# Performance work log

Hardware: AMD Instinct MI355X
Metric: run time of the kernel (lower is better)

## Reference

```python
import jax, jax.numpy as jnp
import numpy as np
from jax import lax

BATCH = 2
COUNT = 5
OUT = 125


def _bins(n, out=OUT):
    # PyTorch adaptive_max_pool2d bin boundaries: start=floor(i*n/out), end=ceil((i+1)*n/out)
    i = np.arange(out)
    s = (i * n) // out
    e = -((-(i + 1) * n) // out)
    m = int((e - s).max())
    idx = s[:, None] + np.arange(m)[None, :]
    return np.minimum(idx, n - 1), idx < e[:, None]


def _apool(img):
    # adaptive max pool 2d of [H,W] -> [OUT,OUT]; H,W are concrete Python ints
    H, W = img.shape
    ri, rv = _bins(H)
    ci, cv = _bins(W)
    r = jnp.where(rv[:, :, None], img[ri], -jnp.inf).max(axis=1)       # [OUT, W]
    return jnp.where(cv[None], r[:, ci], -jnp.inf).max(axis=2)         # [OUT, OUT]


def _conv(x, w, b):
    y = lax.conv_general_dilated(x, w, (1, 1), 'VALID', dimension_numbers=('NCHW', 'OIHW', 'NCHW'))
    return y + b[None, :, None, None]


def _bn(x, g, be, m, v):
    inv = g * lax.rsqrt(v + 1e-5)
    return x * inv[None, :, None, None] + (be - m * inv)[None, :, None, None]


def _pool(x, k, s):
    return lax.reduce_window(x, -np.inf, lax.max, (1, 1, k, k), (1, 1, s, s), 'VALID')


def _forward(x, ROI, roi_layer, w1, b1, g1, be1, m1, v1, w2, b2, g2, be2, m2, v2,
             w3, b3, g3, be3, m3, v3, w4, b4, g4, be4, m4, v4, fw1, fb1, fw2, fb2, fw3, fb3):
    ROI = np.asarray(ROI)
    rl = int(roi_layer)
    roiX = jax.nn.relu(_bn(_conv(x, w1, b1), g1, be1, m1, v1))  # [2,3,252,252]
    crops = []
    for k in range(BATCH):
        xs = []
        for j in range(rl):
            for i in range(COUNT):
                y1, y2, x1, x2 = (int(v) for v in ROI[k, i, 0])
                y1 = int(y1 * 0.9); y2 = int(y2 * 0.9); x2 = int(x2 * 0.9); x1 = int(x1 * 0.9)
                xs.append(_apool(roiX[k, j, y1:y2, x1:x2]))
        crops.append(xs)
    # original code prepends each batch's crop list -> batch order reversed; .numpy() detaches grads
    xb = lax.stop_gradient(jnp.stack(crops[1] + crops[0]).reshape(BATCH, COUNT * rl, OUT, OUT))
    norX = _pool(jax.nn.relu(_bn(_conv(x, w2, b2), g2, be2, m2, v2)), 4, 2)  # [2,20,125,125]
    h = jnp.concatenate([norX, xb], axis=1)                                   # [2,35,125,125]
    h = _pool(jax.nn.relu(_bn(_conv(h, w3, b3), g3, be3, m3, v3)), 2, 2)      # [2,50,60,60]
    h = _pool(jax.nn.relu(_bn(_conv(h, w4, b4), g4, be4, m4, v4)), 2, 2)      # [2,25,28,28]
    h = h.reshape(BATCH, -1)                                                  # [2,19600]
    h = jax.nn.relu(h @ fw1 + fb1)
    h = jax.nn.relu(h @ fw2 + fb2)
    h = jax.nn.relu(h @ fw3 + fb3)
    return jax.nn.softmax(h, axis=1)


def setup_inputs() -> dict:
    key = jax.random.key(0)
    ks = jax.random.split(key, 8)
    rng = np.random.default_rng(0)
    y1 = rng.integers(0, 100, (BATCH, COUNT))
    y2 = np.minimum(y1 + rng.integers(60, 150, (BATCH, COUNT)), 251)
    x1 = rng.integers(0, 100, (BATCH, COUNT))
    x2 = np.minimum(x1 + rng.integers(60, 150, (BATCH, COUNT)), 251)
    ROI = jnp.asarray(np.stack([y1, y2, x1, x2], -1)[:, :, None, :].astype(np.int32))
    d = {'x': jax.random.normal(ks[0], (BATCH, 1, 256, 256), jnp.float32), 'ROI': ROI, 'roi_layer': 3}
    d.update(w1=jax.random.normal(ks[1], (3, 1, 5, 5)) * 0.05, b1=jnp.zeros(3), g1=jnp.ones(3), be1=jnp.zeros(3), m1=jnp.zeros(3), v1=jnp.ones(3))
    d.update(w2=jax.random.normal(ks[2], (20, 1, 5, 5)) * 0.05, b2=jnp.zeros(20), g2=jnp.ones(20), be2=jnp.zeros(20), m2=jnp.zeros(20), v2=jnp.ones(20))
    d.update(w3=jax.random.normal(ks[3], (50, 35, 5, 5)) * 0.05, b3=jnp.zeros(50), g3=jnp.ones(50), be3=jnp.zeros(50), m3=jnp.zeros(50), v3=jnp.ones(50))
    d.update(w4=jax.random.normal(ks[4], (25, 50, 5, 5)) * 0.05, b4=jnp.zeros(25), g4=jnp.ones(25), be4=jnp.zeros(25), m4=jnp.zeros(25), v4=jnp.ones(25))
    d.update(fw1=jax.random.normal(ks[5], (25 * 28 * 28, 1024)) * 0.01, fb1=jnp.zeros(1024),
             fw2=jax.random.normal(ks[6], (1024, 32)) * 0.05, fb2=jnp.zeros(32),
             fw3=jax.random.normal(ks[7], (32, 2)) * 0.05, fb3=jnp.zeros(2))
    return d


def reference(x, ROI, roi_layer, w1, b1, g1, be1, m1, v1, w2, b2, g2, be2, m2, v2,
              w3, b3, g3, be3, m3, v3, w4, b4, g4, be4, m4, v4, fw1, fb1, fw2, fb2, fw3, fb3):
    return _forward(x, ROI, roi_layer, w1, b1, g1, be1, m1, v1, w2, b2, g2, be2, m2, v2,
                    w3, b3, g3, be3, m3, v3, w4, b4, g4, be4, m4, v4, fw1, fb1, fw2, fb2, fw3, fb3)
```

## Files before the change

kernel.cpp:

```cpp
#include <hip/hip_runtime.h>
#include <math.h>


#define RL 3
#define NCH 35

__global__ __launch_bounds__(256) void conv2_roi(
    const float* __restrict__ x, const int* __restrict__ ROI,
    const float* __restrict__ w2, const float* __restrict__ b2, const float* __restrict__ g2,
    const float* __restrict__ be2, const float* __restrict__ m2, const float* __restrict__ v2,
    const float* __restrict__ w1, const float* __restrict__ b1, const float* __restrict__ g1,
    const float* __restrict__ be1, const float* __restrict__ m1, const float* __restrict__ v1,
    float* __restrict__ h1) {
    int i = blockIdx.x * 256 + threadIdx.x;
    if (i >= 125 * 125) return;
    int oy = i / 125, ox = i % 125;
    if (blockIdx.y < 40) {
        int c = blockIdx.y % 20;
        int bi = blockIdx.y / 20;
        const float* xp = x + bi * 256 * 256 + (2 * oy) * 256 + 2 * ox;
        float wl[25];
#pragma unroll
        for (int k = 0; k < 25; k++) wl[k] = w2[c * 25 + k];
        float in[8][8];
#pragma unroll
        for (int r = 0; r < 8; r++)
#pragma unroll
            for (int k = 0; k < 4; k++) {
                float2 v2v = *(const float2*)(xp + r * 256 + 2 * k);
                in[r][2 * k] = v2v.x;
                in[r][2 * k + 1] = v2v.y;
            }
        float inv = g2[c] * rsqrtf(v2[c] + 1e-5f);
        float sh = (b2[c] - m2[c]) * inv + be2[c];
        float mx = -INFINITY;
#pragma unroll
        for (int py = 0; py < 4; py++) {
#pragma unroll
            for (int px = 0; px < 4; px++) {
                float acc = 0.f;
#pragma unroll
                for (int ky = 0; ky < 5; ky++)
#pragma unroll
                    for (int kx = 0; kx < 5; kx++)
                        acc = fmaf(in[py + ky][px + kx], wl[ky * 5 + kx], acc);
                mx = fmaxf(mx, fmaxf(acc * inv + sh, 0.f));
            }
        }
        h1[((bi * NCH + c) * 125 + oy) * 125 + ox] = mx;
    } else {
        int yz = blockIdx.y - 40;
        int bi = yz / 15;
        int cc = yz % 15;
        int sb = 1 - bi;
        int j = cc / 5;
        int ri = cc % 5;
        const int* rp = ROI + (sb * 5 + ri) * 4;
        int y1 = (9 * rp[0]) / 10;
        int y2 = (9 * rp[1]) / 10;
        int x1 = (9 * rp[2]) / 10;
        int x2 = (9 * rp[3]) / 10;
        int H = y2 - y1;
        int W = x2 - x1;
        int sy = (oy * H) / 125, ey = ((oy + 1) * H + 124) / 125;
        int sx = (ox * W) / 125, ex = ((ox + 1) * W + 124) / 125;
        float wl[25];
#pragma unroll
        for (int k = 0; k < 25; k++) wl[k] = w1[j * 25 + k];
        float inv = g1[j] * rsqrtf(v1[j] + 1e-5f);
        float sh = (b1[j] - m1[j]) * inv + be1[j];
        const float* xp = x + sb * 256 * 256;
        float mx = -INFINITY;
        for (int r = sy; r < ey; r++) {
            for (int c2 = sx; c2 < ex; c2++) {
                int Y = y1 + r, X = x1 + c2;
                float acc = 0.f;
#pragma unroll
                for (int ky = 0; ky < 5; ky++)
#pragma unroll
                    for (int kx = 0; kx < 5; kx++)
                        acc = fmaf(xp[(Y + ky) * 256 + X + kx], wl[ky * 5 + kx], acc);
                mx = fmaxf(mx, fmaxf(acc * inv + sh, 0.f));
            }
        }
        h1[((bi * NCH + 20 + cc) * 125 + oy) * 125 + ox] = mx;
    }
}

template <int IW, int PO, int CI, int CO, int G, int NG, int NS>
__global__ __launch_bounds__(64) void conv_partial(
    const float* __restrict__ in, const float* __restrict__ w,
    float* __restrict__ pac) {
    __shared__ float tile[2][20][24];

    const int lane = threadIdx.x;
    const int sy = lane >> 3, sx = lane & 7;
    int z = blockIdx.z;
    const int ng = z % NG; z /= NG;
    const int s = z % NS;
    const int bi = z / NS;
    const int co0 = ng * G;
    constexpr int CPS = (CI + NS - 1) / NS;
    const int ci0 = s * CPS;
    const int ci1 = (ci0 + CPS < CI) ? ci0 + CPS : CI;
    const int px0 = (8 * (int)blockIdx.x < PO - 8) ? 8 * (int)blockIdx.x : PO - 8;
    const int py0 = (8 * (int)blockIdx.y < PO - 8) ? 8 * (int)blockIdx.y : PO - 8;
    const int px = px0 + sx, py = py0 + sy;
    const float* ip = in + (size_t)bi * CI * IW * IW + (size_t)(2 * py0) * IW + 2 * px0;

    int cw[G];
#pragma unroll
    for (int gg = 0; gg < G; gg++) cw[gg] = (co0 + gg < CO) ? co0 + gg : CO - 1;

    float2 sreg[4];
    auto loadstage = [&](int ci) {
        const float* src = ip + (size_t)ci * IW * IW;
#pragma unroll
        for (int k = 0; k < 4; k++) {
            int p = lane + k * 64;
            if (p < 200) {
                int r = p / 10, c2 = (p % 10) * 2;
                sreg[k] = *(const float2*)(src + r * IW + c2);
            }
        }
    };
    auto writestage = [&](int buf) {
#pragma unroll
        for (int k = 0; k < 4; k++) {
            int p = lane + k * 64;
            if (p < 200) {
                int r = p / 10, c2 = (p % 10) * 2;
                *(float2*)&tile[buf][r][c2] = sreg[k];
            }
        }
    };

    loadstage(ci0);
    writestage(0);
    float acc[G][4];
#pragma unroll
    for (int gg = 0; gg < G; gg++)
#pragma unroll
        for (int q = 0; q < 4; q++) acc[gg][q] = 0.f;

    for (int ci = ci0; ci < ci1; ci++) {
        const int cur = (ci - ci0) & 1;
        if (ci + 1 < ci1) loadstage(ci + 1);
        float2 p[6][3];
#pragma unroll
        for (int r = 0; r < 6; r++)
#pragma unroll
            for (int c = 0; c < 3; c++)
                p[r][c] = *(const float2*)&tile[cur][2 * sy + r][2 * sx + 2 * c];
#define E(r, cc) (((cc) & 1) ? p[r][(cc) >> 1].y : p[r][(cc) >> 1].x)
#pragma unroll
        for (int gg = 0; gg < G; gg++) {
            const float* wk = w + ((size_t)cw[gg] * CI + ci) * 25;
#pragma unroll
            for (int ky = 0; ky < 5; ky++) {
#pragma unroll
                for (int kx = 0; kx < 5; kx++) {
                    float wv = wk[ky * 5 + kx];
                    acc[gg][0] = fmaf(E(ky, kx), wv, acc[gg][0]);
                    acc[gg][1] = fmaf(E(ky, kx + 1), wv, acc[gg][1]);
                    acc[gg][2] = fmaf(E(ky + 1, kx), wv, acc[gg][2]);
                    acc[gg][3] = fmaf(E(ky + 1, kx + 1), wv, acc[gg][3]);
                }
            }
        }
#undef E
        if (ci + 1 < ci1) writestage(cur ^ 1);
    }

    constexpr int CW = 2 * PO;
#pragma unroll
    for (int gg = 0; gg < G; gg++) {
        int co = co0 + gg;
        if (co < CO) {
            size_t base = (((size_t)(s * 2 + bi) * CO + co) * CW + 2 * py) * CW + 2 * px;
            float2 r0 = {acc[gg][0], acc[gg][1]};
            float2 r1 = {acc[gg][2], acc[gg][3]};
            *(float2*)&pac[base] = r0;
            *(float2*)&pac[base + CW] = r1;
        }
    }
}

template <int PO, int CO, int NS, int INIT>
__global__ __launch_bounds__(256) void conv_finish(
    const float* __restrict__ pac,
    const float* __restrict__ b, const float* __restrict__ g,
    const float* __restrict__ be, const float* __restrict__ m,
    const float* __restrict__ v, float* __restrict__ out,
    const float* __restrict__ fb1, float* __restrict__ fc1o) {
    int idx = blockIdx.x * 256 + threadIdx.x;
    if (INIT && idx < 2048) fc1o[idx] = fb1[idx & 1023];
    int total = 2 * CO * PO * PO;
    if (idx >= total) return;
    int px = idx % PO;
    int t = idx / PO;
    int py = t % PO; t /= PO;
    int co = t % CO;
    int bi = t / CO;
    constexpr int CW = 2 * PO;
    constexpr size_t SS = (size_t)2 * CO * CW * CW;
    size_t base = (((size_t)bi * CO + co) * CW + 2 * py) * CW + 2 * px;
    float s00 = 0.f, s01 = 0.f, s10 = 0.f, s11 = 0.f;
#pragma unroll
    for (int s = 0; s < NS; s++) {
        float2 a0 = *(const float2*)&pac[base + s * SS];
        float2 a1 = *(const float2*)&pac[base + s * SS + CW];
        s00 += a0.x; s01 += a0.y; s10 += a1.x; s11 += a1.y;
    }
    float inv = g[co] * rsqrtf(v[co] + 1e-5f);
    float sh = (b[co] - m[co]) * inv + be[co];
    float q0 = fmaxf(s00 * inv + sh, 0.f);
    float q1 = fmaxf(s01 * inv + sh, 0.f);
    float q2 = fmaxf(s10 * inv + sh, 0.f);
    float q3 = fmaxf(s11 * inv + sh, 0.f);
    out[idx] = fmaxf(fmaxf(q0, q1), fmaxf(q2, q3));
}

#define CHUNK 50
__global__ void fc1_mm(const float* __restrict__ h, const float* __restrict__ w,
                       float* __restrict__ out) {
    __shared__ float sh[2][CHUNK];
    int o = blockIdx.x * 256 + threadIdx.x;
    int i0 = blockIdx.y * CHUNK;
    if (threadIdx.x < 2 * CHUNK) {
        int r = threadIdx.x / CHUNK, t = threadIdx.x % CHUNK;
        sh[r][t] = h[r * 19600 + i0 + t];
    }
    __syncthreads();
    float a0 = 0.f, a1 = 0.f;
    const float* wp = w + (size_t)i0 * 1024 + o;
#pragma unroll
    for (int i = 0; i < CHUNK; i++) {
        float wv = wp[(size_t)i * 1024];
        a0 = fmaf(sh[0][i], wv, a0);
        a1 = fmaf(sh[1][i], wv, a1);
    }
    atomicAdd(&out[o], a0);
    atomicAdd(&out[1024 + o], a1);
}

__global__ void head(const float* __restrict__ fc1o, const float* __restrict__ fw2,
                     const float* __restrict__ fb2, const float* __restrict__ fw3,
                     const float* __restrict__ fb3, float* __restrict__ out) {
    int bi = blockIdx.x;
    __shared__ float h[1024];
    __shared__ float red[256];
    __shared__ float s2[32];
    for (int i = threadIdx.x; i < 1024; i += 256) h[i] = fmaxf(fc1o[bi * 1024 + i], 0.f);
    __syncthreads();
    int o = threadIdx.x >> 3;
    int part = threadIdx.x & 7;
    float a = 0.f;
    for (int i = part * 128; i < part * 128 + 128; i++) a += h[i] * fw2[i * 32 + o];
    red[threadIdx.x] = a;
    __syncthreads();
    if (part == 0) {
        float s = 0.f;
        for (int p = 0; p < 8; p++) s += red[(o << 3) + p];
        s2[o] = fmaxf(s + fb2[o], 0.f);
    }
    __syncthreads();
    if (threadIdx.x == 0) {
        float z0 = fb3[0], z1 = fb3[1];
        for (int i = 0; i < 32; i++) {
            z0 += s2[i] * fw3[i * 2];
            z1 += s2[i] * fw3[i * 2 + 1];
        }
        z0 = fmaxf(z0, 0.f);
        z1 = fmaxf(z1, 0.f);
        float mx = fmaxf(z0, z1);
        float e0 = expf(z0 - mx), e1 = expf(z1 - mx);
        float s = e0 + e1;
        out[bi * 2 + 0] = e0 / s;
        out[bi * 2 + 1] = e1 / s;
    }
}

extern "C" void kernel_launch(void* const* d_in, const int* in_sizes, int n_in,
                              void* d_out, int out_size, void* d_ws, size_t ws_size,
                              hipStream_t stream) {
    const float* x   = (const float*)d_in[0];
    const int*   ROI = (const int*)d_in[1];
    const float* w1 = (const float*)d_in[3];
    const float* b1 = (const float*)d_in[4];
    const float* g1 = (const float*)d_in[5];
    const float* be1 = (const float*)d_in[6];
    const float* m1 = (const float*)d_in[7];
    const float* v1 = (const float*)d_in[8];
    const float* w2 = (const float*)d_in[9];
    const float* b2 = (const float*)d_in[10];
    const float* g2 = (const float*)d_in[11];
    const float* be2 = (const float*)d_in[12];
    const float* m2 = (const float*)d_in[13];
    const float* v2 = (const float*)d_in[14];
    const float* w3 = (const float*)d_in[15];
    const float* b3 = (const float*)d_in[16];
    const float* g3 = (const float*)d_in[17];
    const float* be3 = (const float*)d_in[18];
    const float* m3 = (const float*)d_in[19];
    const float* v3 = (const float*)d_in[20];
    const float* w4 = (const float*)d_in[21];
    const float* b4 = (const float*)d_in[22];
    const float* g4 = (const float*)d_in[23];
    const float* be4 = (const float*)d_in[24];
    const float* m4 = (const float*)d_in[25];
    const float* v4 = (const float*)d_in[26];
    const float* fw1 = (const float*)d_in[27];
    const float* fb1 = (const float*)d_in[28];
    const float* fw2 = (const float*)d_in[29];
    const float* fb2 = (const float*)d_in[30];
    const float* fw3 = (const float*)d_in[31];
    const float* fb3 = (const float*)d_in[32];
    float* out = (float*)d_out;

    float* ws = (float*)d_ws;
    float* h1   = ws;
    float* p3   = h1 + 1093750;
    float* p4   = p3 + 360000;
    float* fc1o = p4 + 39200;
    float* pac3 = fc1o + 2048;
    float* pac4 = pac3;

    const size_t fixed = 1093750 + 360000 + 39200 + 2048;
    const bool big = ws_size >= (fixed + (size_t)4 * 2 * 50 * 120 * 120) * 4;

    {
        dim3 grd((125 * 125 + 255) / 256, 70);
        conv2_roi<<<grd, 256, 0, stream>>>(x, ROI, w2, b2, g2, be2, m2, v2,
                                           w1, b1, g1, be1, m1, v1, h1);
    }
    if (big) {
        dim3 grd(8, 8, 2 * 4 * 13);
        conv_partial<125, 60, NCH, 50, 4, 13, 4><<<grd, 64, 0, stream>>>(h1, w3, pac3);
        int total = 2 * 50 * 60 * 60;
        conv_finish<60, 50, 4, 0><<<(total + 255) / 256, 256, 0, stream>>>(
            pac3, b3, g3, be3, m3, v3, p3, nullptr, nullptr);
    } else {
        dim3 grd(8, 8, 2 * 2 * 13);
        conv_partial<125, 60, NCH, 50, 4, 13, 2><<<grd, 64, 0, stream>>>(h1, w3, pac3);
        int total = 2 * 50 * 60 * 60;
        conv_finish<60, 50, 2, 0><<<(total + 255) / 256, 256, 0, stream>>>(
            pac3, b3, g3, be3, m3, v3, p3, nullptr, nullptr);
    }
    {
        dim3 grd(4, 4, 2 * 4 * 13);
        conv_partial<60, 28, 50, 25, 2, 13, 4><<<grd, 64, 0, stream>>>(p3, w4, pac4);
    }
    {
        int total = 2 * 25 * 28 * 28;
        conv_finish<28, 25, 4, 1><<<(total + 255) / 256, 256, 0, stream>>>(
            pac4, b4, g4, be4, m4, v4, p4, fb1, fc1o);
    }
    {
        dim3 grd(4, 392);
        fc1_mm<<<grd, 256, 0, stream>>>(p4, fw1, fc1o);
    }
    head<<<2, 256, 0, stream>>>(fc1o, fw2, fb2, fw3, fb3, out);
}
```

Measured before the change: 119.1 us.

## Unroll conv channel loop by two with dual staging registers and rebalance groups

```diff
diff --git a/kernel.cpp b/kernel.cpp
--- a/kernel.cpp
+++ b/kernel.cpp
@@ -112,8 +112,8 @@
 #pragma unroll
     for (int gg = 0; gg < G; gg++) cw[gg] = (co0 + gg < CO) ? co0 + gg : CO - 1;
 
-    float2 sreg[4];
-    auto loadstage = [&](int ci) {
+    float2 sregA[4], sregB[4];
+    auto loadstage = [&](float2(&sreg)[4], int ci) {
         const float* src = ip + (size_t)ci * IW * IW;
 #pragma unroll
         for (int k = 0; k < 4; k++) {
@@ -124,7 +124,7 @@
             }
         }
     };
-    auto writestage = [&](int buf) {
+    auto writestage = [&](int buf, float2(&sreg)[4]) {
 #pragma unroll
         for (int k = 0; k < 4; k++) {
             int p = lane + k * 64;
@@ -135,42 +135,52 @@
         }
     };
 
-    loadstage(ci0);
-    writestage(0);
     float acc[G][4];
 #pragma unroll
     for (int gg = 0; gg < G; gg++)
 #pragma unroll
         for (int q = 0; q < 4; q++) acc[gg][q] = 0.f;
 
-    for (int ci = ci0; ci < ci1; ci++) {
-        const int cur = (ci - ci0) & 1;
-        if (ci + 1 < ci1) loadstage(ci + 1);
-        float2 p[6][3];
-#pragma unroll
-        for (int r = 0; r < 6; r++)
-#pragma unroll
-            for (int c = 0; c < 3; c++)
-                p[r][c] = *(const float2*)&tile[cur][2 * sy + r][2 * sx + 2 * c];
-#define E(r, cc) (((cc) & 1) ? p[r][(cc) >> 1].y : p[r][(cc) >> 1].x)
-#pragma unroll
-        for (int gg = 0; gg < G; gg++) {
-            const float* wk = w + ((size_t)cw[gg] * CI + ci) * 25;
-#pragma unroll
-            for (int ky = 0; ky < 5; ky++) {
-#pragma unroll
-                for (int kx = 0; kx < 5; kx++) {
-                    float wv = wk[ky * 5 + kx];
-                    acc[gg][0] = fmaf(E(ky, kx), wv, acc[gg][0]);
-                    acc[gg][1] = fmaf(E(ky, kx + 1), wv, acc[gg][1]);
-                    acc[gg][2] = fmaf(E(ky + 1, kx), wv, acc[gg][2]);
-                    acc[gg][3] = fmaf(E(ky + 1, kx + 1), wv, acc[gg][3]);
-                }
-            }
-        }
-#undef E
-        if (ci + 1 < ci1) writestage(cur ^ 1);
-    }
+#define FMARND(buf, ci)                                                        \
+    {                                                                          \
+        float2 p[6][3];                                                        \
+        _Pragma("unroll") for (int r = 0; r < 6; r++)                          \
+            _Pragma("unroll") for (int c = 0; c < 3; c++)                      \
+                p[r][c] = *(const float2*)&tile[buf][2 * sy + r][2 * sx + 2 * c]; \
+        _Pragma("unroll") for (int gg = 0; gg < G; gg++) {                     \
+            const float* wk = w + ((size_t)cw[gg] * CI + (ci)) * 25;           \
+            _Pragma("unroll") for (int ky = 0; ky < 5; ky++) {                 \
+                _Pragma("unroll") for (int kx = 0; kx < 5; kx++) {             \
+                    float wv = wk[ky * 5 + kx];                                \
+                    float e00 = ((kx)&1) ? p[ky][kx >> 1].y : p[ky][kx >> 1].x; \
+                    float e01 = ((kx + 1) & 1) ? p[ky][(kx + 1) >> 1].y : p[ky][(kx + 1) >> 1].x; \
+                    float e10 = ((kx)&1) ? p[ky + 1][kx >> 1].y : p[ky + 1][kx >> 1].x; \
+                    float e11 = ((kx + 1) & 1) ? p[ky + 1][(kx + 1) >> 1].y : p[ky + 1][(kx + 1) >> 1].x; \
+                    acc[gg][0] = fmaf(e00, wv, acc[gg][0]);                    \
+                    acc[gg][1] = fmaf(e01, wv, acc[gg][1]);                    \
+                    acc[gg][2] = fmaf(e10, wv, acc[gg][2]);                    \
+                    acc[gg][3] = fmaf(e11, wv, acc[gg][3]);                    \
+                }                                                              \
+            }                                                                  \
+        }                                                                      \
+    }
+
+    loadstage(sregA, ci0);
+    writestage(0, sregA);
+    if (ci0 + 1 < ci1) loadstage(sregA, ci0 + 1);
+
+#pragma unroll 1
+    for (int ci = ci0; ci < ci1; ci += 2) {
+        if (ci + 2 < ci1) loadstage(sregB, ci + 2);
+        FMARND(0, ci);
+        if (ci + 1 < ci1) writestage(1, sregA);
+        if (ci + 1 < ci1) {
+            if (ci + 3 < ci1) loadstage(sregA, ci + 3);
+            FMARND(1, ci + 1);
+            if (ci + 2 < ci1) writestage(0, sregB);
+        }
+    }
+#undef FMARND
 
     constexpr int CW = 2 * PO;
 #pragma unroll
@@ -186,7 +196,7 @@
     }
 }
 
-template <int PO, int CO, int NS, int INIT>
+template <int PO, int CO, int INIT>
 __global__ __launch_bounds__(256) void conv_finish(
     const float* __restrict__ pac,
     const float* __restrict__ b, const float* __restrict__ g,
@@ -207,7 +217,7 @@
     size_t base = (((size_t)bi * CO + co) * CW + 2 * py) * CW + 2 * px;
     float s00 = 0.f, s01 = 0.f, s10 = 0.f, s11 = 0.f;
 #pragma unroll
-    for (int s = 0; s < NS; s++) {
+    for (int s = 0; s < 4; s++) {
         float2 a0 = *(const float2*)&pac[base + s * SS];
         float2 a1 = *(const float2*)&pac[base + s * SS + CW];
         s00 += a0.x; s01 += a0.y; s10 += a1.x; s11 += a1.y;
@@ -326,34 +336,27 @@
     float* pac3 = fc1o + 2048;
     float* pac4 = pac3;
 
-    const size_t fixed = 1093750 + 360000 + 39200 + 2048;
-    const bool big = ws_size >= (fixed + (size_t)4 * 2 * 50 * 120 * 120) * 4;
-
     {
         dim3 grd((125 * 125 + 255) / 256, 70);
         conv2_roi<<<grd, 256, 0, stream>>>(x, ROI, w2, b2, g2, be2, m2, v2,
                                            w1, b1, g1, be1, m1, v1, h1);
     }
-    if (big) {
-        dim3 grd(8, 8, 2 * 4 * 13);
-        conv_partial<125, 60, NCH, 50, 4, 13, 4><<<grd, 64, 0, stream>>>(h1, w3, pac3);
+    {
+        dim3 grd(8, 8, 2 * 4 * 10);
+        conv_partial<125, 60, NCH, 50, 5, 10, 4><<<grd, 64, 0, stream>>>(h1, w3, pac3);
+    }
+    {
         int total = 2 * 50 * 60 * 60;
-        conv_finish<60, 50, 4, 0><<<(total + 255) / 256, 256, 0, stream>>>(
+        conv_finish<60, 50, 0><<<(total + 255) / 256, 256, 0, stream>>>(
             pac3, b3, g3, be3, m3, v3, p3, nullptr, nullptr);
-    } else {
-        dim3 grd(8, 8, 2 * 2 * 13);
-        conv_partial<125, 60, NCH, 50, 4, 13, 2><<<grd, 64, 0, stream>>>(h1, w3, pac3);
-        int total = 2 * 50 * 60 * 60;
-        conv_finish<60, 50, 2, 0><<<(total + 255) / 256, 256, 0, stream>>>(
-            pac3, b3, g3, be3, m3, v3, p3, nullptr, nullptr);
-    }
-    {
-        dim3 grd(4, 4, 2 * 4 * 13);
-        conv_partial<60, 28, 50, 25, 2, 13, 4><<<grd, 64, 0, stream>>>(p3, w4, pac4);
+    }
+    {
+        dim3 grd(4, 4, 2 * 4 * 5);
+        conv_partial<60, 28, 50, 25, 5, 5, 4><<<grd, 64, 0, stream>>>(p3, w4, pac4);
     }
     {
         int total = 2 * 25 * 28 * 28;
-        conv_finish<28, 25, 4, 1><<<(total + 255) / 256, 256, 0, stream>>>(
+        conv_finish<28, 25, 1><<<(total + 255) / 256, 256, 0, stream>>>(
             pac4, b4, g4, be4, m4, v4, p4, fb1, fc1o);
     }
     {
```

Result: slower. 130.3 us (+9.4%).
